# Performance work log

Hardware: AMD Instinct MI355X
Metric: run time of the kernel (lower is better)

Reference implementation:

```python
import jax, jax.numpy as jnp
import numpy as np

K = 1024
H = 16

def setup_inputs() -> dict:
    key = jax.random.key(0)
    ks = jax.random.split(key, 6)
    s = 1.0 / np.sqrt(K)
    return {
        "x": jax.random.normal(ks[0], (2, 2048, K), dtype=jnp.float32),
        "Wq": jax.random.uniform(ks[1], (K, K), jnp.float32, -s, s),
        "Wk": jax.random.uniform(ks[2], (K, K), jnp.float32, -s, s),
        "Wv": jax.random.uniform(ks[3], (K, K), jnp.float32, -s, s),
        "Wu": jax.random.uniform(ks[4], (K, K), jnp.float32, -s, s),
        "bu": jax.random.uniform(ks[5], (K,), jnp.float32, -s, s),
    }

def reference(x, Wq, Wk, Wv, Wu, bu):
    b, t, k = x.shape
    hd = k // H  # head dim = 64
    scale = jnp.asarray(k, x.dtype) ** 0.25  # Bloem-style: scale q and k each by k^(1/4)
    # nn.Linear(bias=False): y = x @ W.T
    q = (jnp.einsum('btk,ok->bto', x, Wq) / scale).reshape(b, t, H, hd)
    kk = (jnp.einsum('btk,ok->bto', x, Wk) / scale).reshape(b, t, H, hd)
    v = jnp.einsum('btk,ok->bto', x, Wv).reshape(b, t, H, hd)
    dot = jnp.einsum('bthd,bshd->bhts', q, kk)  # [b,h,t,t]
    att = jax.nn.softmax(dot, axis=-1)
    out = jnp.einsum('bhts,bshd->bthd', att, v).reshape(b, t, k)
    return jnp.einsum('btk,ok->bto', out, Wu) + bu
```

## Files before the change

kernel.cpp:

```cpp
#include <hip/hip_runtime.h>

typedef __bf16 bf16;
typedef bf16  bf16x8 __attribute__((ext_vector_type(8)));
typedef bf16  bf16x4 __attribute__((ext_vector_type(4)));
typedef float f32x4  __attribute__((ext_vector_type(4)));

#define MFMA16(a, b, c) __builtin_amdgcn_mfma_f32_16x16x32_bf16((a), (b), (c), 0, 0, 0)
#define AS1 __attribute__((address_space(1)))
#define AS3 __attribute__((address_space(3)))

__device__ __forceinline__ void gld_lds16(const bf16* g, bf16* l) {
    __builtin_amdgcn_global_load_lds((AS1 void*)(g), (AS3 void*)(l), 16, 0, 0);
}

__global__ __launch_bounds__(256) void cvt_f32_bf16(const float* __restrict__ src,
                                                    bf16* __restrict__ dst, float scale) {
    int idx = (blockIdx.x * 256 + threadIdx.x) * 4;
    float4 v = *(const float4*)(src + idx);
    bf16x4 o;
    o[0] = (bf16)(v.x * scale); o[1] = (bf16)(v.y * scale);
    o[2] = (bf16)(v.z * scale); o[3] = (bf16)(v.w * scale);
    *(bf16x4*)(dst + idx) = o;
}

__device__ __forceinline__ void gemm_core(const bf16* __restrict__ A, const bf16* __restrict__ B,
                                          int mBase, int nBase, bf16* As, bf16* Bs,
                                          f32x4 acc[4][4]) {
    const int tid = threadIdx.x;
    const int wave = tid >> 6, lane = tid & 63;
    const int g = lane >> 4, lr = lane & 15;
    const int wm = (wave & 1) << 6, wn = (wave >> 1) << 6;

    int off0 = (wave << 10) + (lane << 4);
    int row0 = off0 >> 6,            col0 = (off0 & 63) >> 1;
    int off1 = off0 + 4096;
    int row1 = off1 >> 6,            col1 = (off1 & 63) >> 1;
    int ldsA0 = (wave << 9), ldsA1 = ldsA0 + 2048;

    for (int k0 = 0; k0 < 1024; k0 += 32) {
        __syncthreads();
        gld_lds16(A + (size_t)(mBase + row0) * 1024 + k0 + col0, As + ldsA0);
        gld_lds16(A + (size_t)(mBase + row1) * 1024 + k0 + col1, As + ldsA1);
        gld_lds16(B + (size_t)(nBase + row0) * 1024 + k0 + col0, Bs + ldsA0);
        gld_lds16(B + (size_t)(nBase + row1) * 1024 + k0 + col1, Bs + ldsA1);
        __syncthreads();

        bf16x8 af[4], bfr[4];
#pragma unroll
        for (int i = 0; i < 4; i++)
            af[i] = *(const bf16x8*)&As[(wm + (i << 4) + lr) * 32 + (g << 3)];
#pragma unroll
        for (int j = 0; j < 4; j++)
            bfr[j] = *(const bf16x8*)&Bs[(wn + (j << 4) + lr) * 32 + (g << 3)];
#pragma unroll
        for (int i = 0; i < 4; i++)
#pragma unroll
            for (int j = 0; j < 4; j++)
                acc[i][j] = MFMA16(af[i], bfr[j], acc[i][j]);
    }
}

__global__ __launch_bounds__(256) void gemm_qkv(const bf16* __restrict__ A,
                                                const bf16* __restrict__ Wq, const bf16* __restrict__ Wk,
                                                const bf16* __restrict__ Wv,
                                                bf16* __restrict__ Qo, bf16* __restrict__ Ko,
                                                bf16* __restrict__ Vto) {
    __shared__ bf16 As[128 * 32];
    __shared__ bf16 Bs[128 * 32];
    const int tid = threadIdx.x;
    const int wave = tid >> 6, lane = tid & 63;
    const int g = lane >> 4, lr = lane & 15;
    const int wm = (wave & 1) << 6, wn = (wave >> 1) << 6;
    const int z = blockIdx.z;

    const bf16 *Ap, *Bp;
    int mBase, nBase;
    if (z == 2) { Ap = Wv; Bp = A;                 mBase = blockIdx.x * 128; nBase = blockIdx.y * 128; }
    else        { Ap = A;  Bp = z ? Wk : Wq;       mBase = blockIdx.y * 128; nBase = blockIdx.x * 128; }

    f32x4 acc[4][4] = {};
    gemm_core(Ap, Bp, mBase, nBase, As, Bs, acc);

#pragma unroll
    for (int i = 0; i < 4; i++)
#pragma unroll
        for (int j = 0; j < 4; j++)
#pragma unroll
            for (int r = 0; r < 4; r++) {
                int m = mBase + wm + (i << 4) + (g << 2) + r;
                int n = nBase + wn + (j << 4) + lr;
                bf16 v = (bf16)acc[i][j][r];
                if (z == 2) {
                    int h = m >> 6, d = m & 63, b = n >> 11, t = n & 2047;
                    Vto[((size_t)(((b << 4) + h) << 6) + d) * 2048 + t] = v;
                } else {
                    int b = m >> 11, t = m & 2047, h = n >> 6, d = n & 63;
                    bf16* dst = (z == 0) ? Qo : Ko;
                    dst[(((size_t)((b << 4) + h) * 2048 + t) << 6) + d] = v;
                }
            }
}

__global__ __launch_bounds__(256) void gemm_out(const bf16* __restrict__ A, const bf16* __restrict__ B,
                                                const float* __restrict__ bias, float* __restrict__ out) {
    __shared__ bf16 As[128 * 32];
    __shared__ bf16 Bs[128 * 32];
    const int tid = threadIdx.x;
    const int wave = tid >> 6, lane = tid & 63;
    const int g = lane >> 4, lr = lane & 15;
    const int wm = (wave & 1) << 6, wn = (wave >> 1) << 6;
    const int mBase = blockIdx.y * 128, nBase = blockIdx.x * 128;

    f32x4 acc[4][4] = {};
    gemm_core(A, B, mBase, nBase, As, Bs, acc);

#pragma unroll
    for (int i = 0; i < 4; i++)
#pragma unroll
        for (int j = 0; j < 4; j++) {
            int n = nBase + wn + (j << 4) + lr;
            float bv = bias[n];
#pragma unroll
            for (int r = 0; r < 4; r++) {
                int m = mBase + wm + (i << 4) + (g << 2) + r;
                out[((size_t)m << 10) + n] = acc[i][j][r] + bv;
            }
        }
}

__global__ __launch_bounds__(256) void attn(const bf16* __restrict__ Q, const bf16* __restrict__ Kt,
                                            const bf16* __restrict__ Vt, bf16* __restrict__ O) {
    __shared__ bf16 Qs[2][128][32];
    __shared__ bf16 Ks[2][128][32];
    __shared__ bf16 Vs[4][64][32];
    bf16 (*Ps)[32][32] = (bf16(*)[32][32]) & Qs[0][0][0];

    const int tid = threadIdx.x;
    const int wave = tid >> 6, lane = tid & 63;
    const int g = lane >> 4, lr = lane & 15;
    const int bh = blockIdx.y;
    const int qBase = blockIdx.x << 7;

    const bf16* Qg = Q + ((size_t)bh * 2048 + qBase) * 64;
    const bf16* Kg = Kt + (size_t)bh * 2048 * 64;
    const bf16* Vg = Vt + (size_t)bh * 64 * 2048;

#pragma unroll
    for (int i = 0; i < 4; i++) {
        int bi = (wave << 2) + i;
        int p = bi >> 3, rb = (bi & 7) << 4;
        int r = rb + (lane >> 2), c = (lane & 3) << 3;
        gld_lds16(Qg + r * 64 + (p << 5) + c, &Qs[p][rb][0]);
    }
    __syncthreads();

    bf16x8 qf[2][2];
#pragma unroll
    for (int ks = 0; ks < 2; ks++)
#pragma unroll
        for (int tt = 0; tt < 2; tt++)
            qf[ks][tt] = *(const bf16x8*)&Qs[ks][(wave << 5) + (tt << 4) + lr][g << 3];

    f32x4 oacc[2][4] = {};
    float lsum[2] = {0.f, 0.f};

    for (int s0 = 0; s0 < 2048; s0 += 128) {
        __syncthreads();
#pragma unroll
        for (int i = 0; i < 4; i++) {
            int bi = (wave << 2) + i;
            {
                int p = bi >> 3, rb = (bi & 7) << 4;
                int r = rb + (lane >> 2), c = (lane & 3) << 3;
                gld_lds16(Kg + (size_t)(s0 + r) * 64 + (p << 5) + c, &Ks[p][rb][0]);
            }
            {
                int p = bi >> 2, rb = (bi & 3) << 4;
                int r = rb + (lane >> 2), c = (lane & 3) << 3;
                gld_lds16(Vg + (size_t)r * 2048 + s0 + (p << 5) + c, &Vs[p][rb][0]);
            }
        }
        __syncthreads();

#pragma unroll
        for (int ks2 = 0; ks2 < 4; ks2++) {
            f32x4 sacc[2][2] = {};
#pragma unroll
            for (int isub = 0; isub < 2; isub++) {
                int is = (ks2 << 1) + isub;
#pragma unroll
                for (int ks = 0; ks < 2; ks++) {
                    bf16x8 kf = *(const bf16x8*)&Ks[ks][(is << 4) + lr][g << 3];
                    sacc[isub][0] = MFMA16(kf, qf[ks][0], sacc[isub][0]);
                    sacc[isub][1] = MFMA16(kf, qf[ks][1], sacc[isub][1]);
                }
            }
#pragma unroll
            for (int isub = 0; isub < 2; isub++)
#pragma unroll
                for (int tt = 0; tt < 2; tt++) {
                    f32x4 s = sacc[isub][tt];
                    float e0 = __builtin_amdgcn_exp2f(s[0]);
                    float e1 = __builtin_amdgcn_exp2f(s[1]);
                    float e2 = __builtin_amdgcn_exp2f(s[2]);
                    float e3 = __builtin_amdgcn_exp2f(s[3]);
                    lsum[tt] += (e0 + e1) + (e2 + e3);
                    bf16x4 pb;
                    pb[0] = (bf16)e0; pb[1] = (bf16)e1; pb[2] = (bf16)e2; pb[3] = (bf16)e3;
                    *(bf16x4*)&Ps[wave][(tt << 4) + lr][(isub << 4) + (g << 2)] = pb;
                }
            __asm__ volatile("s_waitcnt lgkmcnt(0)" ::: "memory");

            bf16x8 pf0 = *(const bf16x8*)&Ps[wave][lr][g << 3];
            bf16x8 pf1 = *(const bf16x8*)&Ps[wave][16 + lr][g << 3];
#pragma unroll
            for (int jd = 0; jd < 4; jd++) {
                bf16x8 vf = *(const bf16x8*)&Vs[ks2][(jd << 4) + lr][g << 3];
                oacc[0][jd] = MFMA16(pf0, vf, oacc[0][jd]);
                oacc[1][jd] = MFMA16(pf1, vf, oacc[1][jd]);
            }
        }
    }

#pragma unroll
    for (int tt = 0; tt < 2; tt++) {
        lsum[tt] += __shfl_xor(lsum[tt], 16, 64);
        lsum[tt] += __shfl_xor(lsum[tt], 32, 64);
    }
    float linv[2][4];
#pragma unroll
    for (int tt = 0; tt < 2; tt++)
#pragma unroll
        for (int r = 0; r < 4; r++)
            linv[tt][r] = 1.0f / __shfl(lsum[tt], (g << 2) + r, 64);

    const int b = bh >> 4, h = bh & 15;
#pragma unroll
    for (int tt = 0; tt < 2; tt++)
#pragma unroll
        for (int jd = 0; jd < 4; jd++)
#pragma unroll
            for (int r = 0; r < 4; r++) {
                int t = qBase + (wave << 5) + (tt << 4) + (g << 2) + r;
                int col = (h << 6) + (jd << 4) + lr;
                O[(((size_t)(b * 2048 + t)) << 10) + col] = (bf16)(oacc[tt][jd][r] * linv[tt][r]);
            }
}

extern "C" void kernel_launch(void* const* d_in, const int* in_sizes, int n_in,
                              void* d_out, int out_size, void* d_ws, size_t ws_size,
                              hipStream_t stream) {
    const float* x  = (const float*)d_in[0];
    const float* Wq = (const float*)d_in[1];
    const float* Wk = (const float*)d_in[2];
    const float* Wv = (const float*)d_in[3];
    const float* Wu = (const float*)d_in[4];
    const float* bu = (const float*)d_in[5];
    float* out = (float*)d_out;

    char* ws = (char*)d_ws;
    bf16* xbf  = (bf16*)(ws);
    bf16* wqbf = (bf16*)(ws + ((size_t)8  << 20));
    bf16* wkbf = (bf16*)(ws + ((size_t)10 << 20));
    bf16* wvbf = (bf16*)(ws + ((size_t)12 << 20));
    bf16* wubf = (bf16*)(ws + ((size_t)14 << 20));
    bf16* Qb   = (bf16*)(ws + ((size_t)16 << 20));
    bf16* Kb   = (bf16*)(ws + ((size_t)24 << 20));
    bf16* Vtb  = (bf16*)(ws + ((size_t)32 << 20));
    bf16* attnO = xbf;

    const float iscale_k = 0.17677669529663687f;
    const float iscale_q = 0.25503540109f;

    cvt_f32_bf16<<<4096, 256, 0, stream>>>(x,  xbf,  1.0f);
    cvt_f32_bf16<<<1024, 256, 0, stream>>>(Wq, wqbf, iscale_q);
    cvt_f32_bf16<<<1024, 256, 0, stream>>>(Wk, wkbf, iscale_k);
    cvt_f32_bf16<<<1024, 256, 0, stream>>>(Wv, wvbf, 1.0f);
    cvt_f32_bf16<<<1024, 256, 0, stream>>>(Wu, wubf, 1.0f);

    gemm_qkv<<<dim3(8, 32, 3), 256, 0, stream>>>(xbf, wqbf, wkbf, wvbf, Qb, Kb, Vtb);
    attn<<<dim3(16, 32), 256, 0, stream>>>(Qb, Kb, Vtb, attnO);
    gemm_out<<<dim3(8, 32), 256, 0, stream>>>(attnO, wubf, bu, out);
}
```

Baseline: 222.2 us.

## XOR-swizzle LDS tiles in GEMM and attention, merge weight conversion launches

Applies an XOR swizzle to the column chunk position when global_load_lds writes A/B, Q, K, V and P tiles into LDS, with matching swizzled read offsets. This is meant to remove LDS bank conflicts on the bf16x8 fragment reads. The four weight conversion launches are merged into one 2D-grid kernel to cut launch overhead. The explicit lgkmcnt wait before reading P back is removed, which relies on the compiler to order the LDS store and load and risks a hazard if it does not.

```diff
diff --git a/kernel.cpp b/kernel.cpp
--- a/kernel.cpp
+++ b/kernel.cpp
@@ -13,13 +13,31 @@
     __builtin_amdgcn_global_load_lds((AS1 void*)(g), (AS3 void*)(l), 16, 0, 0);
 }
 
-__global__ __launch_bounds__(256) void cvt_f32_bf16(const float* __restrict__ src,
-                                                    bf16* __restrict__ dst, float scale) {
+
+__global__ __launch_bounds__(256) void cvt_x(const float* __restrict__ src, bf16* __restrict__ dst) {
     int idx = (blockIdx.x * 256 + threadIdx.x) * 4;
     float4 v = *(const float4*)(src + idx);
     bf16x4 o;
-    o[0] = (bf16)(v.x * scale); o[1] = (bf16)(v.y * scale);
-    o[2] = (bf16)(v.z * scale); o[3] = (bf16)(v.w * scale);
+    o[0] = (bf16)v.x; o[1] = (bf16)v.y; o[2] = (bf16)v.z; o[3] = (bf16)v.w;
+    *(bf16x4*)(dst + idx) = o;
+}
+
+__global__ __launch_bounds__(256) void cvt_weights(const float* __restrict__ Wq, const float* __restrict__ Wk,
+                                                   const float* __restrict__ Wv, const float* __restrict__ Wu,
+                                                   bf16* oq, bf16* ok, bf16* ov, bf16* ou,
+                                                   float sq, float sk) {
+    const float* src; bf16* dst; float sc;
+    switch (blockIdx.y) {
+        case 0:  src = Wq; dst = oq; sc = sq;   break;
+        case 1:  src = Wk; dst = ok; sc = sk;   break;
+        case 2:  src = Wv; dst = ov; sc = 1.0f; break;
+        default: src = Wu; dst = ou; sc = 1.0f; break;
+    }
+    int idx = (blockIdx.x * 256 + threadIdx.x) * 4;
+    float4 v = *(const float4*)(src + idx);
+    bf16x4 o;
+    o[0] = (bf16)(v.x * sc); o[1] = (bf16)(v.y * sc);
+    o[2] = (bf16)(v.z * sc); o[3] = (bf16)(v.w * sc);
     *(bf16x4*)(dst + idx) = o;
 }
 
@@ -30,28 +48,31 @@
     const int wave = tid >> 6, lane = tid & 63;
     const int g = lane >> 4, lr = lane & 15;
     const int wm = (wave & 1) << 6, wn = (wave >> 1) << 6;
-
-    int off0 = (wave << 10) + (lane << 4);
-    int row0 = off0 >> 6,            col0 = (off0 & 63) >> 1;
-    int off1 = off0 + 4096;
-    int row1 = off1 >> 6,            col1 = (off1 & 63) >> 1;
-    int ldsA0 = (wave << 9), ldsA1 = ldsA0 + 2048;
+    const int q = lane >> 2;
+    const int cswz = ((lane & 3) ^ ((lane >> 3) & 3)) << 3;
+    const int pcs  = (g ^ ((lr >> 1) & 3)) << 3;
+
+    const int rb0 = wave << 4, rb1 = rb0 + 64;
+    const bf16* a0 = A + (size_t)(mBase + rb0 + q) * 1024 + cswz;
+    const bf16* a1 = A + (size_t)(mBase + rb1 + q) * 1024 + cswz;
+    const bf16* b0 = B + (size_t)(nBase + rb0 + q) * 1024 + cswz;
+    const bf16* b1 = B + (size_t)(nBase + rb1 + q) * 1024 + cswz;
 
     for (int k0 = 0; k0 < 1024; k0 += 32) {
         __syncthreads();
-        gld_lds16(A + (size_t)(mBase + row0) * 1024 + k0 + col0, As + ldsA0);
-        gld_lds16(A + (size_t)(mBase + row1) * 1024 + k0 + col1, As + ldsA1);
-        gld_lds16(B + (size_t)(nBase + row0) * 1024 + k0 + col0, Bs + ldsA0);
-        gld_lds16(B + (size_t)(nBase + row1) * 1024 + k0 + col1, Bs + ldsA1);
+        gld_lds16(a0 + k0, As + rb0 * 32);
+        gld_lds16(a1 + k0, As + rb1 * 32);
+        gld_lds16(b0 + k0, Bs + rb0 * 32);
+        gld_lds16(b1 + k0, Bs + rb1 * 32);
         __syncthreads();
 
         bf16x8 af[4], bfr[4];
 #pragma unroll
         for (int i = 0; i < 4; i++)
-            af[i] = *(const bf16x8*)&As[(wm + (i << 4) + lr) * 32 + (g << 3)];
+            af[i] = *(const bf16x8*)&As[(wm + (i << 4) + lr) * 32 + pcs];
 #pragma unroll
         for (int j = 0; j < 4; j++)
-            bfr[j] = *(const bf16x8*)&Bs[(wn + (j << 4) + lr) * 32 + (g << 3)];
+            bfr[j] = *(const bf16x8*)&Bs[(wn + (j << 4) + lr) * 32 + pcs];
 #pragma unroll
         for (int i = 0; i < 4; i++)
 #pragma unroll
@@ -75,8 +96,8 @@
 
     const bf16 *Ap, *Bp;
     int mBase, nBase;
-    if (z == 2) { Ap = Wv; Bp = A;                 mBase = blockIdx.x * 128; nBase = blockIdx.y * 128; }
-    else        { Ap = A;  Bp = z ? Wk : Wq;       mBase = blockIdx.y * 128; nBase = blockIdx.x * 128; }
+    if (z == 2) { Ap = Wv; Bp = A;            mBase = blockIdx.x * 128; nBase = blockIdx.y * 128; }
+    else        { Ap = A;  Bp = z ? Wk : Wq;  mBase = blockIdx.y * 128; nBase = blockIdx.x * 128; }
 
     f32x4 acc[4][4] = {};
     gemm_core(Ap, Bp, mBase, nBase, As, Bs, acc);
@@ -138,6 +159,12 @@
     const int tid = threadIdx.x;
     const int wave = tid >> 6, lane = tid & 63;
     const int g = lane >> 4, lr = lane & 15;
+    const int q = lane >> 2;
+    const int cswz = ((lane & 3) ^ ((lane >> 3) & 3)) << 3;
+    const int pcs  = (g ^ ((lr >> 1) & 3)) << 3;
+    const int pw0 = ((((g >> 1))     ^ ((lr >> 1) & 3)) << 3) + ((g & 1) << 2);
+    const int pw1 = (((2 + (g >> 1)) ^ ((lr >> 1) & 3)) << 3) + ((g & 1) << 2);
+
     const int bh = blockIdx.y;
     const int qBase = blockIdx.x << 7;
 
@@ -149,8 +176,7 @@
     for (int i = 0; i < 4; i++) {
         int bi = (wave << 2) + i;
         int p = bi >> 3, rb = (bi & 7) << 4;
-        int r = rb + (lane >> 2), c = (lane & 3) << 3;
-        gld_lds16(Qg + r * 64 + (p << 5) + c, &Qs[p][rb][0]);
+        gld_lds16(Qg + (rb + q) * 64 + (p << 5) + cswz, &Qs[p][rb][0]);
     }
     __syncthreads();
 
@@ -159,7 +185,7 @@
     for (int ks = 0; ks < 2; ks++)
 #pragma unroll
         for (int tt = 0; tt < 2; tt++)
-            qf[ks][tt] = *(const bf16x8*)&Qs[ks][(wave << 5) + (tt << 4) + lr][g << 3];
+            qf[ks][tt] = *(const bf16x8*)&Qs[ks][(wave << 5) + (tt << 4) + lr][pcs];
 
     f32x4 oacc[2][4] = {};
     float lsum[2] = {0.f, 0.f};
@@ -171,13 +197,11 @@
             int bi = (wave << 2) + i;
             {
                 int p = bi >> 3, rb = (bi & 7) << 4;
-                int r = rb + (lane >> 2), c = (lane & 3) << 3;
-                gld_lds16(Kg + (size_t)(s0 + r) * 64 + (p << 5) + c, &Ks[p][rb][0]);
+                gld_lds16(Kg + (size_t)(s0 + rb + q) * 64 + (p << 5) + cswz, &Ks[p][rb][0]);
             }
             {
                 int p = bi >> 2, rb = (bi & 3) << 4;
-                int r = rb + (lane >> 2), c = (lane & 3) << 3;
-                gld_lds16(Vg + (size_t)r * 2048 + s0 + (p << 5) + c, &Vs[p][rb][0]);
+                gld_lds16(Vg + (size_t)(rb + q) * 2048 + s0 + (p << 5) + cswz, &Vs[p][rb][0]);
             }
         }
         __syncthreads();
@@ -190,7 +214,7 @@
                 int is = (ks2 << 1) + isub;
 #pragma unroll
                 for (int ks = 0; ks < 2; ks++) {
-                    bf16x8 kf = *(const bf16x8*)&Ks[ks][(is << 4) + lr][g << 3];
+                    bf16x8 kf = *(const bf16x8*)&Ks[ks][(is << 4) + lr][pcs];
                     sacc[isub][0] = MFMA16(kf, qf[ks][0], sacc[isub][0]);
                     sacc[isub][1] = MFMA16(kf, qf[ks][1], sacc[isub][1]);
                 }
@@ -207,15 +231,13 @@
                     lsum[tt] += (e0 + e1) + (e2 + e3);
                     bf16x4 pb;
                     pb[0] = (bf16)e0; pb[1] = (bf16)e1; pb[2] = (bf16)e2; pb[3] = (bf16)e3;
-                    *(bf16x4*)&Ps[wave][(tt << 4) + lr][(isub << 4) + (g << 2)] = pb;
+                    *(bf16x4*)&Ps[wave][(tt << 4) + lr][isub ? pw1 : pw0] = pb;
                 }
-            __asm__ volatile("s_waitcnt lgkmcnt(0)" ::: "memory");
-
-            bf16x8 pf0 = *(const bf16x8*)&Ps[wave][lr][g << 3];
-            bf16x8 pf1 = *(const bf16x8*)&Ps[wave][16 + lr][g << 3];
+            bf16x8 pf0 = *(const bf16x8*)&Ps[wave][lr][pcs];
+            bf16x8 pf1 = *(const bf16x8*)&Ps[wave][16 + lr][pcs];
 #pragma unroll
             for (int jd = 0; jd < 4; jd++) {
-                bf16x8 vf = *(const bf16x8*)&Vs[ks2][(jd << 4) + lr][g << 3];
+                bf16x8 vf = *(const bf16x8*)&Vs[ks2][(jd << 4) + lr][pcs];
                 oacc[0][jd] = MFMA16(pf0, vf, oacc[0][jd]);
                 oacc[1][jd] = MFMA16(pf1, vf, oacc[1][jd]);
             }
@@ -272,11 +294,9 @@
     const float iscale_k = 0.17677669529663687f;
     const float iscale_q = 0.25503540109f;
 
-    cvt_f32_bf16<<<4096, 256, 0, stream>>>(x,  xbf,  1.0f);
-    cvt_f32_bf16<<<1024, 256, 0, stream>>>(Wq, wqbf, iscale_q);
-    cvt_f32_bf16<<<1024, 256, 0, stream>>>(Wk, wkbf, iscale_k);
-    cvt_f32_bf16<<<1024, 256, 0, stream>>>(Wv, wvbf, 1.0f);
-    cvt_f32_bf16<<<1024, 256, 0, stream>>>(Wu, wubf, 1.0f);
+    cvt_x<<<4096, 256, 0, stream>>>(x, xbf);
+    cvt_weights<<<dim3(1024, 4), 256, 0, stream>>>(Wq, Wk, Wv, Wu, wqbf, wkbf, wvbf, wubf,
+                                                   iscale_q, iscale_k);
 
     gemm_qkv<<<dim3(8, 32, 3), 256, 0, stream>>>(xbf, wqbf, wkbf, wvbf, Qb, Kb, Vtb);
     attn<<<dim3(16, 32), 256, 0, stream>>>(Qb, Kb, Vtb, attnO);
```

After: 200.4 us. 9.8% less time.
